# Kernel tuning notes

Hardware: AMD Instinct MI355X
Metric: run time of the kernel (lower is better)

## Reference

```python
import jax, jax.numpy as jnp
import numpy as np

C = 768
TEMB = 512
HID = int(C * 2.0)  # prompt_mlp hidden
K = max(1, int(C * 0.5))  # top-k channels = 384


def silu(x):
    return x * jax.nn.sigmoid(x)


def conv1x1(h, W, b):
    # h: [b,c,H,W], W: [o,c], b: [o]
    return jnp.einsum('bchw,oc->bohw', h, W) + b[None, :, None, None]


def setup_inputs() -> dict:
    key = jax.random.key(0)
    ks = jax.random.split(key, 20)
    s = 0.02
    return {
        'x': jax.random.normal(ks[0], (16, C, 64, 64), jnp.float32),
        'temb': jax.random.normal(ks[1], (16, TEMB), jnp.float32),
        'W_ts': jax.random.normal(ks[2], (2 * C, TEMB), jnp.float32) * s,
        'b_ts': jnp.zeros((2 * C,), jnp.float32),
        'W_tp': jax.random.normal(ks[3], (C, TEMB), jnp.float32) * s,
        'b_tp': jnp.zeros((C,), jnp.float32),
        'W_m1': jax.random.normal(ks[4], (HID, 2 * C), jnp.float32) * s,
        'b_m1': jnp.zeros((HID,), jnp.float32),
        'W_m2': jax.random.normal(ks[5], (C, HID), jnp.float32) * s,
        'b_m2': jnp.zeros((C,), jnp.float32),
        'Wq': jax.random.normal(ks[6], (C, C), jnp.float32) * s,
        'bq': jnp.zeros((C,), jnp.float32),
        'Wk': jax.random.normal(ks[7], (C, C), jnp.float32) * s,
        'bk': jnp.zeros((C,), jnp.float32),
        'Wv': jax.random.normal(ks[8], (C, C), jnp.float32) * s,
        'bv': jnp.zeros((C,), jnp.float32),
        'Wo': jax.random.normal(ks[9], (C, C), jnp.float32) * s,
        'bo': jnp.zeros((C,), jnp.float32),
    }


def reference(x, temb, W_ts, b_ts, W_tp, b_tp, W_m1, b_m1, W_m2, b_m2,
              Wq, bq, Wk, bk, Wv, bv, Wo, bo):
    b, c, H, W = x.shape
    # TimeScaleShift
    ss = silu(temb) @ W_ts.T + b_ts                       # [b, 2c]
    scale, shift = jnp.split(ss, 2, axis=1)
    h = x * (1 + scale[:, :, None, None]) + shift[:, :, None, None]
    # prompt
    gap = h.mean(axis=(2, 3))                             # [b, c]
    tp = silu(temb) @ W_tp.T + b_tp                       # [b, c]
    p = jnp.concatenate([gap, tp], axis=1)                # [b, 2c]
    prompt = silu(p @ W_m1.T + b_m1) @ W_m2.T + b_m2      # [b, c]
    # top-k channel selection
    _, idx = jax.lax.top_k(prompt, K)                     # [b, K]
    bi = jnp.arange(b)[:, None]
    # 1x1 convs then gather selected channels
    q = conv1x1(h, Wq, bq)[bi, idx].reshape(b, K, H * W)
    kf = conv1x1(h, Wk, bk)[bi, idx].reshape(b, K, H * W)
    v = conv1x1(h, Wv, bv)[bi, idx].reshape(b, K, H * W)
    # channel attention
    attn = jax.nn.softmax(jnp.einsum('bkn,bln->bkl', q, kf) * (K ** -0.5), axis=-1)
    out = jnp.einsum('bkl,bln->bkn', attn, v).reshape(b, K, H, W)
    # scatter back into full channel space
    out_full = jnp.zeros_like(h).at[bi, idx].set(out)
    return conv1x1(out_full, Wo, bo)
```

## Files before the change

### kernel.cpp

```cpp
#include <hip/hip_runtime.h>

#define NB 16
#define NC 768
#define NT 512
#define KS 384
#define NPX 4096
#define BK 64

typedef __bf16 bfx8 __attribute__((ext_vector_type(8)));
typedef float fx4 __attribute__((ext_vector_type(4)));
typedef unsigned short u16;
typedef unsigned short usv4 __attribute__((ext_vector_type(4)));

__device__ __forceinline__ u16 f2bf(float f) {
  unsigned u = __builtin_bit_cast(unsigned, f);
  u += 0x7FFFu + ((u >> 16) & 1u);
  return (u16)(u >> 16);
}
__device__ __forceinline__ float bf2f(u16 v) {
  return __builtin_bit_cast(float, (unsigned)v << 16);
}

__device__ __forceinline__ void gload16(const u16* g, u16* l) {
  __builtin_amdgcn_global_load_lds(
      (const __attribute__((address_space(1))) unsigned int*)g,
      (__attribute__((address_space(3))) unsigned int*)l, 16, 0, 0);
}

__global__ void k_trans_mean(const float* __restrict__ x, u16* __restrict__ xT,
                             u16* __restrict__ xC, float* __restrict__ parts) {
  __shared__ float ld[64][65];
  int p0 = blockIdx.x * 64, c0 = blockIdx.y * 64, b = blockIdx.z;
  int t = threadIdx.x;
  int k = t & 15, ir = t >> 4;
  int jr = k * 4;
#pragma unroll
  for (int s = 0; s < 4; ++s) {
    int i = ir + s * 16;
    float4 v = *(const float4*)&x[(size_t)(b * NC + c0 + i) * NPX + p0 + jr];
    ld[i][jr] = v.x; ld[i][jr + 1] = v.y; ld[i][jr + 2] = v.z; ld[i][jr + 3] = v.w;
    usv4 pk = {f2bf(v.x), f2bf(v.y), f2bf(v.z), f2bf(v.w)};
    *(usv4*)&xC[(size_t)(b * NC + c0 + i) * NPX + p0 + jr] = pk;
  }
  __syncthreads();
#pragma unroll
  for (int s = 0; s < 4; ++s) {
    int j = ir + s * 16;
    usv4 pk = {f2bf(ld[k * 4][j]), f2bf(ld[k * 4 + 1][j]),
               f2bf(ld[k * 4 + 2][j]), f2bf(ld[k * 4 + 3][j])};
    *(usv4*)&xT[(size_t)(b * NPX + p0 + j) * NC + c0 + k * 4] = pk;
  }
  if (t < 64) {
    float s = 0.f;
    for (int j = 0; j < 64; ++j) s += ld[t][j];
    parts[(size_t)(b * NC + c0 + t) * 64 + blockIdx.x] = s;
  }
}

__global__ void k_misc(const float* __restrict__ parts, float* __restrict__ xmean,
                       const float* __restrict__ temb, float* __restrict__ st) {
  int id = blockIdx.x * 256 + threadIdx.x;
  if (id < NB * NT) { float v = temb[id]; st[id] = v / (1.f + expf(-v)); }
  if (id < NB * NC) {
    float s = 0.f;
    for (int j = 0; j < 64; ++j) s += parts[(size_t)id * 64 + j];
    xmean[id] = s * (1.f / 4096.f);
  }
}

__global__ void k_mlp8(const float* __restrict__ W, const float* __restrict__ bias,
                       const float* __restrict__ X, float* __restrict__ Y,
                       int len, int nj, int ostride, int obase, int dosilu) {
  __shared__ float Xs[8 * 1537];
  int t = threadIdx.x, lane = t & 63, w = t >> 6;
  int b0 = blockIdx.y * 8;
  int ldx = len + 1;
  for (int id = t; id < 8 * len; id += 256) {
    int bb = id / len, s = id - bb * len;
    Xs[bb * ldx + s] = X[(size_t)(b0 + bb) * len + s];
  }
  __syncthreads();
  for (int i = 0; i < 4; ++i) {
    int j = blockIdx.x * 16 + i * 4 + w;
    if (j < nj) {
      float acc[8] = {0, 0, 0, 0, 0, 0, 0, 0};
      for (int s = lane; s < len; s += 64) {
        float wv = W[(size_t)j * len + s];
#pragma unroll
        for (int bb = 0; bb < 8; ++bb) acc[bb] += wv * Xs[bb * ldx + s];
      }
#pragma unroll
      for (int bb = 0; bb < 8; ++bb) {
        float r = acc[bb];
#pragma unroll
        for (int m = 32; m; m >>= 1) r += __shfl_xor(r, m);
        if (lane == 0) {
          r += bias[j];
          if (dosilu) r = r / (1.f + expf(-r));
          Y[(size_t)(b0 + bb) * ostride + obase + j] = r;
        }
      }
    }
  }
}

__global__ void k_assemble_p(const float* __restrict__ Y1, const float* __restrict__ xmean,
                             float* __restrict__ p) {
  int id = blockIdx.x * 256 + threadIdx.x;
  if (id >= NB * NC) return;
  int b = id / NC, c = id - b * NC;
  const float* yb = Y1 + (size_t)b * 2304;
  p[(size_t)b * 1536 + c] = xmean[id] * (1.f + yb[c]) + yb[768 + c];
  p[(size_t)b * 1536 + 768 + c] = yb[1536 + c];
}

__global__ void k_topk(const float* __restrict__ prompt, int* __restrict__ idx) {
  __shared__ float pr[NC];
  int b = blockIdx.x, t = threadIdx.x;
  for (int c = t; c < NC; c += 256) pr[c] = prompt[(size_t)b * NC + c];
  __syncthreads();
  for (int c = t; c < NC; c += 256) {
    float v = pr[c];
    int r = 0;
    for (int c2 = 0; c2 < NC; ++c2) {
      float v2 = pr[c2];
      r += (v2 > v) || (v2 == v && c2 < c);
    }
    if (r < KS) idx[b * KS + r] = c;
  }
}

__global__ void k_fold(const int* __restrict__ idx, const float* __restrict__ Y1,
                       const float* __restrict__ xmean,
                       const float* __restrict__ Wq, const float* __restrict__ bq,
                       const float* __restrict__ Wk, const float* __restrict__ bk,
                       const float* __restrict__ Wv, const float* __restrict__ bv,
                       u16* __restrict__ Aq, u16* __restrict__ Avtmp,
                       float* __restrict__ biasq, float* __restrict__ sig) {
  __shared__ float red[5 * 256];
  int k = blockIdx.x, b = blockIdx.y, t = threadIdx.x;
  int row = idx[b * KS + k];
  const float* yb = Y1 + (size_t)b * 2304;
  u16* aq = Aq + (size_t)b * 768 * NC;
  u16* av = Avtmp + (size_t)b * KS * NC;
  float dq = 0.f, dk = 0.f, dv = 0.f, sq = 0.f, sk = 0.f;
  for (int c = t; c < NC; c += 256) {
    float sc = 1.f + yb[c], sh = yb[768 + c];
    float xm = xmean[b * NC + c];
    float wq = Wq[(size_t)row * NC + c];
    float wk = Wk[(size_t)row * NC + c];
    float wv = Wv[(size_t)row * NC + c];
    aq[(size_t)k * NC + c] = f2bf(wq * sc);
    aq[(size_t)(KS + k) * NC + c] = f2bf(wk * sc);
    av[(size_t)k * NC + c] = f2bf(wv * sc);
    dq += wq * sh; dk += wk * sh; dv += wv * sh;
    sq += wq * sc * xm; sk += wk * sc * xm;
  }
  red[t] = dq; red[256 + t] = dk; red[512 + t] = dv; red[768 + t] = sq; red[1024 + t] = sk;
  __syncthreads();
  for (int s = 128; s; s >>= 1) {
    if (t < s) {
#pragma unroll
      for (int q = 0; q < 5; ++q) red[q * 256 + t] += red[q * 256 + t + s];
    }
    __syncthreads();
  }
  if (t == 0) {
    biasq[b * 1152 + k] = bq[row] + red[0];
    biasq[b * 1152 + KS + k] = bk[row] + red[256];
    biasq[b * 1152 + 2 * KS + k] = bv[row] + red[512];
    sig[b * NC + k] = 4096.f * red[768];
    sig[b * NC + KS + k] = 4096.f * red[1024];
  }
}

__global__ void k_avt(const u16* __restrict__ Avtmp, u16* __restrict__ AvT) {
  __shared__ u16 tl[64][65];
  int lt = blockIdx.x % 6, ct = blockIdx.x / 6, b = blockIdx.y;
  int l0 = lt * 64, c0 = ct * 64, t = threadIdx.x;
#pragma unroll
  for (int s = 0; s < 16; ++s) {
    int id = t + 256 * s;
    int r = id >> 6, c = id & 63;
    tl[r][c] = Avtmp[(size_t)b * KS * NC + (size_t)(l0 + r) * NC + c0 + c];
  }
  __syncthreads();
#pragma unroll
  for (int s = 0; s < 16; ++s) {
    int id = t + 256 * s;
    int r = id >> 6, c = id & 63;
    AvT[(size_t)b * NC * KS + (size_t)(c0 + r) * KS + l0 + c] = tl[c][r];
  }
}

__global__ void k_gather_wo(const int* __restrict__ idx, const float* __restrict__ Wo,
                            u16* __restrict__ WoSel) {
  __shared__ int il[KS];
  int b = blockIdx.y, t = threadIdx.x;
  for (int k = t; k < KS; k += 256) il[k] = idx[b * KS + k];
  __syncthreads();
  int o0 = blockIdx.x * 8;
  for (int oo = 0; oo < 8; ++oo) {
    int o = o0 + oo;
    const float* wr = Wo + (size_t)o * NC;
    u16* dst = WoSel + ((size_t)b * NC + o) * KS;
    for (int k = t; k < KS; k += 256) dst[k] = f2bf(wr[il[k]]);
  }
}

__global__ void k_gmerge(const float* __restrict__ Gp, u16* __restrict__ G) {
  __shared__ u16 gl[128][130];
  int tt = blockIdx.x, b = blockIdx.y, t = threadIdx.x;
  int i = 0;
  while ((i + 1) * (i + 2) / 2 <= tt) ++i;
  int j = tt - i * (i + 1) / 2;
  const float* p0 = Gp + ((size_t)(0 * NB + b) * 21 + tt) * 16384;
  const float* p1 = Gp + ((size_t)(1 * NB + b) * 21 + tt) * 16384;
#pragma unroll
  for (int s = 0; s < 16; ++s) {
    int id = t + 256 * s;
    int row = id >> 5, col4 = (id & 31) * 4;
    float4 a = *(const float4*)&p0[row * 128 + col4];
    float4 bb = *(const float4*)&p1[row * 128 + col4];
    usv4 pk = {f2bf(a.x + bb.x), f2bf(a.y + bb.y), f2bf(a.z + bb.z), f2bf(a.w + bb.w)};
    gl[row][col4] = pk[0]; gl[row][col4 + 1] = pk[1];
    gl[row][col4 + 2] = pk[2]; gl[row][col4 + 3] = pk[3];
    *(usv4*)&G[((size_t)b * NC + i * 128 + row) * NC + j * 128 + col4] = pk;
  }
  if (i == j) return;
  __syncthreads();
#pragma unroll
  for (int s = 0; s < 16; ++s) {
    int id = t + 256 * s;
    int row = id >> 5, col4 = (id & 31) * 4;
    usv4 pk = {gl[col4][row], gl[col4 + 1][row], gl[col4 + 2][row], gl[col4 + 3][row]};
    *(usv4*)&G[((size_t)b * NC + j * 128 + row) * NC + i * 128 + col4] = pk;
  }
}

__global__ void k_softmax(const float* __restrict__ S, u16* __restrict__ At) {
  __shared__ float sh[2];
  int kk = blockIdx.x, b = blockIdx.y, t = threadIdx.x;
  const float* srow = S + ((size_t)b * KS + kk) * KS;
  float v[3];
#pragma unroll
  for (int i = 0; i < 3; ++i) v[i] = srow[t + 128 * i];
  float m = fmaxf(fmaxf(v[0], v[1]), v[2]);
#pragma unroll
  for (int s = 32; s; s >>= 1) m = fmaxf(m, __shfl_xor(m, s));
  if ((t & 63) == 0) sh[t >> 6] = m;
  __syncthreads();
  m = fmaxf(sh[0], sh[1]);
  float e[3];
  float sum = 0.f;
#pragma unroll
  for (int i = 0; i < 3; ++i) { e[i] = expf(v[i] - m); sum += e[i]; }
#pragma unroll
  for (int s = 32; s; s >>= 1) sum += __shfl_xor(sum, s);
  __syncthreads();
  if ((t & 63) == 0) sh[t >> 6] = sum;
  __syncthreads();
  sum = sh[0] + sh[1];
  float inv = 1.f / sum;
#pragma unroll
  for (int i = 0; i < 3; ++i) {
    int l = t + 128 * i;
    At[((size_t)b * KS + l) * KS + kk] = f2bf(e[i] * inv);
  }
}

__global__ void k_bias_fin(const u16* __restrict__ R, const float* __restrict__ biasq,
                           const float* __restrict__ bo, float* __restrict__ bias_fin) {
  __shared__ float bv[KS];
  int b = blockIdx.x, t = threadIdx.x;
  for (int l = t; l < KS; l += 256) bv[l] = biasq[b * 1152 + 768 + l];
  __syncthreads();
  for (int o = t; o < NC; o += 256) {
    const u16* rr = R + ((size_t)b * NC + o) * KS;
    float s = bo[o];
    for (int l = 0; l < KS; ++l) s += bf2f(rr[l]) * bv[l];
    bias_fin[b * NC + o] = s;
  }
}

template <int EPI>
__global__ __launch_bounds__(256, 2) void gemm_bt(
    const u16* __restrict__ A, const u16* __restrict__ Bt, size_t sA, size_t sB,
    int ldA, int ldB, int K, const float* __restrict__ bias, int bstride,
    float* __restrict__ outF, u16* __restrict__ outU, int ldC, size_t sC,
    const float* __restrict__ sigp, const float* __restrict__ bqp, float scale) {
  __shared__ u16 As[128 * BK];
  __shared__ u16 Bs[128 * BK];
  int b, m0, n0, kbeg = 0, kend = K, tt = 0, gpart = 0;
  if constexpr (EPI == 5) {
    tt = blockIdx.x;
    int ii = 0;
    while ((ii + 1) * (ii + 2) / 2 <= tt) ++ii;
    int jj = tt - ii * (ii + 1) / 2;
    m0 = ii * 128; n0 = jj * 128;
    b = blockIdx.z >> 1; gpart = blockIdx.z & 1;
    kbeg = gpart * 2048; kend = kbeg + 2048;
  } else {
    b = blockIdx.z; m0 = blockIdx.y * 128; n0 = blockIdx.x * 128;
  }
  const u16* Ab = A + (size_t)b * sA;
  const u16* Bb = Bt + (size_t)b * sB;
  int t = threadIdx.x, lane = t & 63, w = t >> 6;
  int wm = (w >> 1) * 64, wn = (w & 1) * 64;
  int r16 = lane & 15, g = lane >> 4;

  int srow = w * 32 + (lane >> 3);
  int scol = (lane & 7) * 8;
  const u16* Ag = Ab + (size_t)(m0 + srow) * ldA + kbeg + scol;
  const u16* Bg = Bb + (size_t)(n0 + srow) * ldB + kbeg + scol;
  u16* Asl = &As[(w * 32) * BK];
  u16* Bsl = &Bs[(w * 32) * BK];

  fx4 acc[4][4] = {};

  for (int k0 = kbeg; k0 < kend; k0 += BK) {
#pragma unroll
    for (int s = 0; s < 4; ++s) gload16(Ag + (size_t)s * 8 * ldA, Asl + s * 8 * BK);
#pragma unroll
    for (int s = 0; s < 4; ++s) gload16(Bg + (size_t)s * 8 * ldB, Bsl + s * 8 * BK);
    Ag += BK; Bg += BK;
    __syncthreads();
#pragma unroll
    for (int kk = 0; kk < 2; ++kk) {
      bfx8 af[4], bfr[4];
#pragma unroll
      for (int i = 0; i < 4; ++i) {
        af[i] = *(const bfx8*)&As[(wm + i * 16 + r16) * BK + kk * 32 + g * 8];
        bfr[i] = *(const bfx8*)&Bs[(wn + i * 16 + r16) * BK + kk * 32 + g * 8];
      }
#pragma unroll
      for (int i = 0; i < 4; ++i)
#pragma unroll
        for (int j = 0; j < 4; ++j)
          acc[i][j] = __builtin_amdgcn_mfma_f32_16x16x32_bf16(af[i], bfr[j], acc[i][j], 0, 0, 0);
    }
    __syncthreads();
  }

#pragma unroll
  for (int i = 0; i < 4; ++i) {
#pragma unroll
    for (int j = 0; j < 4; ++j) {
      int row = wm + i * 16 + g * 4;
      int col = wn + j * 16 + r16;
      fx4 v = acc[i][j];
      if constexpr (EPI == 1) {
        int gc = n0 + col;
        float bk_ = bqp[b * 1152 + 384 + gc];
        float sk_ = sigp[b * NC + 384 + gc];
#pragma unroll
        for (int r = 0; r < 4; ++r) {
          int gr = m0 + row + r;
          float bq_ = bqp[b * 1152 + gr];
          float sq_ = sigp[b * NC + gr];
          float val = (v[r] + bq_ * sk_ + bk_ * sq_ + 4096.f * bq_ * bk_) * scale;
          outF[(size_t)b * sC + (size_t)gr * ldC + gc] = val;
        }
      } else if constexpr (EPI == 2) {
#pragma unroll
        for (int r = 0; r < 4; ++r)
          outU[(size_t)b * sC + (size_t)(m0 + row + r) * ldC + (n0 + col)] = f2bf(v[r]);
      } else if constexpr (EPI == 3) {
#pragma unroll
        for (int r = 0; r < 4; ++r)
          outF[(size_t)b * sC + (size_t)(m0 + row + r) * ldC + (n0 + col)] =
              v[r] + bias[b * bstride + m0 + row + r];
      } else {
        float* o = outF + ((size_t)(gpart * NB + b) * 21 + tt) * 16384;
#pragma unroll
        for (int r = 0; r < 4; ++r) o[(row + r) * 128 + col] = v[r];
      }
    }
  }
}

__global__ void k_sentinel(float* out, int n) {
  int id = blockIdx.x * 256 + threadIdx.x;
  if (id < n) out[id] = 12345.0f;
}

extern "C" void kernel_launch(void* const* d_in, const int* in_sizes, int n_in,
                              void* d_out, int out_size, void* d_ws, size_t ws_size,
                              hipStream_t stream) {
  const float* x    = (const float*)d_in[0];
  const float* temb = (const float*)d_in[1];
  const float* W_ts = (const float*)d_in[2];
  const float* b_ts = (const float*)d_in[3];
  const float* W_tp = (const float*)d_in[4];
  const float* b_tp = (const float*)d_in[5];
  const float* W_m1 = (const float*)d_in[6];
  const float* b_m1 = (const float*)d_in[7];
  const float* W_m2 = (const float*)d_in[8];
  const float* b_m2 = (const float*)d_in[9];
  const float* Wq = (const float*)d_in[10];
  const float* bq = (const float*)d_in[11];
  const float* Wk = (const float*)d_in[12];
  const float* bk = (const float*)d_in[13];
  const float* Wv = (const float*)d_in[14];
  const float* bv = (const float*)d_in[15];
  const float* Wo = (const float*)d_in[16];
  const float* bo = (const float*)d_in[17];
  float* out = (float*)d_out;

  char* base = (char*)d_ws;
  size_t off = 0;
  auto alloc = [&](size_t bytes) -> char* {
    char* pp = base + off;
    off += (bytes + 255) & ~(size_t)255;
    return pp;
  };
  u16* xT   = (u16*)alloc((size_t)NB * NPX * NC * 2);
  u16* xC   = (u16*)alloc((size_t)NB * NC * NPX * 2);
  u16* Aq   = (u16*)alloc((size_t)NB * 768 * NC * 2);
  u16* AvT  = (u16*)alloc((size_t)NB * NC * KS * 2);
  u16* WoS  = (u16*)alloc((size_t)NB * NC * KS * 2);
  float* Gp = (float*)alloc((size_t)2 * NB * 21 * 16384 * 4);
  float* parts  = (float*)alloc((size_t)NB * NC * 64 * 4);
  float* xmean  = (float*)alloc((size_t)NB * NC * 4);
  float* Y1     = (float*)alloc((size_t)NB * 2304 * 4);
  float* st     = (float*)alloc((size_t)NB * NT * 4);
  float* p      = (float*)alloc((size_t)NB * 1536 * 4);
  float* hid    = (float*)alloc((size_t)NB * 1536 * 4);
  float* pr     = (float*)alloc((size_t)NB * NC * 4);
  int*   idx    = (int*)alloc((size_t)NB * KS * 4);
  float* biasq  = (float*)alloc((size_t)NB * 1152 * 4);
  float* sig    = (float*)alloc((size_t)NB * NC * 4);
  float* bias_fin = (float*)alloc((size_t)NB * NC * 4);

  if (off > ws_size) {
    k_sentinel<<<(out_size + 255) / 256, 256, 0, stream>>>(out, out_size);
    return;
  }

  u16* Avtmp = (u16*)Gp;
  u16* G   = (u16*)xC;
  u16* T   = (u16*)((char*)xC + 20u * 1024 * 1024);
  float* S = (float*)((char*)xC + 32u * 1024 * 1024);
  u16* At  = (u16*)((char*)xC + 44u * 1024 * 1024);
  u16* R   = (u16*)((char*)xC + 52u * 1024 * 1024);
  u16* Wf  = (u16*)((char*)xC + 64u * 1024 * 1024);

  k_trans_mean<<<dim3(64, 12, NB), 256, 0, stream>>>(x, xT, xC, parts);
  k_misc<<<48, 256, 0, stream>>>(parts, xmean, temb, st);
  k_mlp8<<<dim3(96, 2), 256, 0, stream>>>(W_ts, b_ts, st, Y1, 512, 1536, 2304, 0, 0);
  k_mlp8<<<dim3(48, 2), 256, 0, stream>>>(W_tp, b_tp, st, Y1, 512, 768, 2304, 1536, 0);
  k_assemble_p<<<(NB * NC + 255) / 256, 256, 0, stream>>>(Y1, xmean, p);
  k_mlp8<<<dim3(96, 2), 256, 0, stream>>>(W_m1, b_m1, p, hid, 1536, 1536, 1536, 0, 1);
  k_mlp8<<<dim3(48, 2), 256, 0, stream>>>(W_m2, b_m2, hid, pr, 1536, 768, 768, 0, 0);
  k_topk<<<NB, 256, 0, stream>>>(pr, idx);
  k_fold<<<dim3(KS, NB), 256, 0, stream>>>(idx, Y1, xmean, Wq, bq, Wk, bk, Wv, bv,
                                           Aq, Avtmp, biasq, sig);
  k_avt<<<dim3(72, NB), 256, 0, stream>>>(Avtmp, AvT);
  k_gather_wo<<<dim3(96, NB), 256, 0, stream>>>(idx, Wo, WoS);

  gemm_bt<5><<<dim3(21, 1, NB * 2), 256, 0, stream>>>(
      xC, xC, (size_t)NC * NPX, (size_t)NC * NPX, NPX, NPX, NPX,
      nullptr, 0, Gp, nullptr, 0, 0, nullptr, nullptr, 0.f);
  k_gmerge<<<dim3(21, NB), 256, 0, stream>>>(Gp, G);
  gemm_bt<2><<<dim3(6, 3, NB), 256, 0, stream>>>(
      Aq + (size_t)KS * NC, G, (size_t)768 * NC, (size_t)NC * NC, NC, NC, NC,
      nullptr, 0, nullptr, T, NC, (size_t)KS * NC, nullptr, nullptr, 0.f);
  gemm_bt<1><<<dim3(3, 3, NB), 256, 0, stream>>>(
      Aq, T, (size_t)768 * NC, (size_t)KS * NC, NC, NC, NC,
      nullptr, 0, S, nullptr, KS, (size_t)KS * KS, sig, biasq, 0.05103103630798287f);
  k_softmax<<<dim3(KS, NB), 128, 0, stream>>>(S, At);
  gemm_bt<2><<<dim3(3, 6, NB), 256, 0, stream>>>(
      WoS, At, (size_t)NC * KS, (size_t)KS * KS, KS, KS, KS,
      nullptr, 0, nullptr, R, KS, (size_t)NC * KS, nullptr, nullptr, 0.f);
  k_bias_fin<<<NB, 256, 0, stream>>>(R, biasq, bo, bias_fin);
  gemm_bt<2><<<dim3(6, 6, NB), 256, 0, stream>>>(
      R, AvT, (size_t)NC * KS, (size_t)NC * KS, KS, KS, KS,
      nullptr, 0, nullptr, Wf, NC, (size_t)NC * NC, nullptr, nullptr, 0.f);
  gemm_bt<3><<<dim3(32, 6, NB), 256, 0, stream>>>(
      Wf, xT, (size_t)NC * NC, (size_t)NPX * NC, NC, NC, NC,
      bias_fin, NC, out, nullptr, NPX, (size_t)NC * NPX, nullptr, nullptr, 0.f);
}
```

Baseline: 684.5 us.

## Fuse prompt MLP chain and top-k into one per-batch kernel

Replaces the silu, four small MLP launches, prompt assembly and top-k with a single 1024-thread kernel per batch element that keeps intermediates in shared memory. It also parallelizes the final-bias reduction across many blocks with wave-level reductions, and raises the GEMM launch-bounds occupancy hint. The fusion removes several launches and global round-trips, but each of the 16 blocks now streams all MLP weights itself, so only 16 CUs work and weight traffic multiplies. The higher occupancy hint may force register spills in the GEMM.

```diff
diff --git a/kernel.cpp b/kernel.cpp
--- a/kernel.cpp
+++ b/kernel.cpp
@@ -57,76 +57,97 @@
   }
 }
 
-__global__ void k_misc(const float* __restrict__ parts, float* __restrict__ xmean,
-                       const float* __restrict__ temb, float* __restrict__ st) {
-  int id = blockIdx.x * 256 + threadIdx.x;
-  if (id < NB * NT) { float v = temb[id]; st[id] = v / (1.f + expf(-v)); }
-  if (id < NB * NC) {
+__global__ __launch_bounds__(1024, 1) void k_prompt(
+    const float* __restrict__ temb, const float* __restrict__ parts,
+    const float* __restrict__ W_ts, const float* __restrict__ b_ts,
+    const float* __restrict__ W_tp, const float* __restrict__ b_tp,
+    const float* __restrict__ W_m1, const float* __restrict__ b_m1,
+    const float* __restrict__ W_m2, const float* __restrict__ b_m2,
+    float* __restrict__ xmean_g, float* __restrict__ Y1, int* __restrict__ idx) {
+  __shared__ float st[512];
+  __shared__ float ssl[2304];
+  __shared__ float pl[1536];
+  __shared__ float hidl[1536];
+  __shared__ float prl[768];
+  __shared__ float xml[768];
+  int b = blockIdx.x, t = threadIdx.x, lane = t & 63, w = t >> 6;
+
+  if (t < 512) { float v = temb[b * 512 + t]; st[t] = v / (1.f + expf(-v)); }
+  if (t < 768) {
+    const float* pp = parts + (size_t)(b * 768 + t) * 64;
     float s = 0.f;
-    for (int j = 0; j < 64; ++j) s += parts[(size_t)id * 64 + j];
-    xmean[id] = s * (1.f / 4096.f);
-  }
-}
-
-__global__ void k_mlp8(const float* __restrict__ W, const float* __restrict__ bias,
-                       const float* __restrict__ X, float* __restrict__ Y,
-                       int len, int nj, int ostride, int obase, int dosilu) {
-  __shared__ float Xs[8 * 1537];
-  int t = threadIdx.x, lane = t & 63, w = t >> 6;
-  int b0 = blockIdx.y * 8;
-  int ldx = len + 1;
-  for (int id = t; id < 8 * len; id += 256) {
-    int bb = id / len, s = id - bb * len;
-    Xs[bb * ldx + s] = X[(size_t)(b0 + bb) * len + s];
-  }
-  __syncthreads();
-  for (int i = 0; i < 4; ++i) {
-    int j = blockIdx.x * 16 + i * 4 + w;
-    if (j < nj) {
-      float acc[8] = {0, 0, 0, 0, 0, 0, 0, 0};
-      for (int s = lane; s < len; s += 64) {
-        float wv = W[(size_t)j * len + s];
-#pragma unroll
-        for (int bb = 0; bb < 8; ++bb) acc[bb] += wv * Xs[bb * ldx + s];
-      }
-#pragma unroll
-      for (int bb = 0; bb < 8; ++bb) {
-        float r = acc[bb];
-#pragma unroll
-        for (int m = 32; m; m >>= 1) r += __shfl_xor(r, m);
-        if (lane == 0) {
-          r += bias[j];
-          if (dosilu) r = r / (1.f + expf(-r));
-          Y[(size_t)(b0 + bb) * ostride + obase + j] = r;
-        }
-      }
-    }
-  }
-}
-
-__global__ void k_assemble_p(const float* __restrict__ Y1, const float* __restrict__ xmean,
-                             float* __restrict__ p) {
-  int id = blockIdx.x * 256 + threadIdx.x;
-  if (id >= NB * NC) return;
-  int b = id / NC, c = id - b * NC;
-  const float* yb = Y1 + (size_t)b * 2304;
-  p[(size_t)b * 1536 + c] = xmean[id] * (1.f + yb[c]) + yb[768 + c];
-  p[(size_t)b * 1536 + 768 + c] = yb[1536 + c];
-}
-
-__global__ void k_topk(const float* __restrict__ prompt, int* __restrict__ idx) {
-  __shared__ float pr[NC];
-  int b = blockIdx.x, t = threadIdx.x;
-  for (int c = t; c < NC; c += 256) pr[c] = prompt[(size_t)b * NC + c];
-  __syncthreads();
-  for (int c = t; c < NC; c += 256) {
-    float v = pr[c];
+    for (int j = 0; j < 64; ++j) s += pp[j];
+    float xm = s * (1.f / 4096.f);
+    xml[t] = xm;
+    xmean_g[b * 768 + t] = xm;
+  }
+  __syncthreads();
+
+  for (int j = w; j < 2304; j += 16) {
+    const float* wr = (j < 1536) ? W_ts + (size_t)j * 512 : W_tp + (size_t)(j - 1536) * 512;
+    float4 a0 = *(const float4*)&wr[lane * 8];
+    float4 a1 = *(const float4*)&wr[lane * 8 + 4];
+    float4 s0 = *(const float4*)&st[lane * 8];
+    float4 s1 = *(const float4*)&st[lane * 8 + 4];
+    float acc = a0.x * s0.x + a0.y * s0.y + a0.z * s0.z + a0.w * s0.w +
+                a1.x * s1.x + a1.y * s1.y + a1.z * s1.z + a1.w * s1.w;
+#pragma unroll
+    for (int m = 32; m; m >>= 1) acc += __shfl_xor(acc, m);
+    if (lane == 0) {
+      acc += (j < 1536) ? b_ts[j] : b_tp[j - 1536];
+      ssl[j] = acc;
+      if (j < 1536) Y1[(size_t)b * 2304 + j] = acc;
+    }
+  }
+  __syncthreads();
+
+  if (t < 768) {
+    pl[t] = xml[t] * (1.f + ssl[t]) + ssl[768 + t];
+    pl[768 + t] = ssl[1536 + t];
+  }
+  __syncthreads();
+
+  for (int j = w; j < 1536; j += 16) {
+    const float* wr = W_m1 + (size_t)j * 1536;
+    float acc = 0.f;
+#pragma unroll
+    for (int e = 0; e < 6; ++e) {
+      float4 a = *(const float4*)&wr[lane * 24 + e * 4];
+      float4 s = *(const float4*)&pl[lane * 24 + e * 4];
+      acc += a.x * s.x + a.y * s.y + a.z * s.z + a.w * s.w;
+    }
+#pragma unroll
+    for (int m = 32; m; m >>= 1) acc += __shfl_xor(acc, m);
+    if (lane == 0) {
+      acc += b_m1[j];
+      hidl[j] = acc / (1.f + expf(-acc));
+    }
+  }
+  __syncthreads();
+
+  for (int j = w; j < 768; j += 16) {
+    const float* wr = W_m2 + (size_t)j * 1536;
+    float acc = 0.f;
+#pragma unroll
+    for (int e = 0; e < 6; ++e) {
+      float4 a = *(const float4*)&wr[lane * 24 + e * 4];
+      float4 s = *(const float4*)&hidl[lane * 24 + e * 4];
+      acc += a.x * s.x + a.y * s.y + a.z * s.z + a.w * s.w;
+    }
+#pragma unroll
+    for (int m = 32; m; m >>= 1) acc += __shfl_xor(acc, m);
+    if (lane == 0) prl[j] = acc + b_m2[j];
+  }
+  __syncthreads();
+
+  if (t < 768) {
+    float v = prl[t];
     int r = 0;
-    for (int c2 = 0; c2 < NC; ++c2) {
-      float v2 = pr[c2];
-      r += (v2 > v) || (v2 == v && c2 < c);
-    }
-    if (r < KS) idx[b * KS + r] = c;
+    for (int c2 = 0; c2 < 768; ++c2) {
+      float v2 = prl[c2];
+      r += (v2 > v) || (v2 == v && c2 < t);
+    }
+    if (r < KS) idx[b * KS + r] = t;
   }
 }
 
@@ -271,20 +292,28 @@
 
 __global__ void k_bias_fin(const u16* __restrict__ R, const float* __restrict__ biasq,
                            const float* __restrict__ bo, float* __restrict__ bias_fin) {
-  __shared__ float bv[KS];
-  int b = blockIdx.x, t = threadIdx.x;
-  for (int l = t; l < KS; l += 256) bv[l] = biasq[b * 1152 + 768 + l];
-  __syncthreads();
-  for (int o = t; o < NC; o += 256) {
+  __shared__ float bvl[KS];
+  int b = blockIdx.y, t = threadIdx.x, lane = t & 63, w = t >> 6;
+  for (int l = t; l < KS; l += 256) bvl[l] = biasq[b * 1152 + 768 + l];
+  __syncthreads();
+  int o0 = blockIdx.x * 16;
+  for (int oo = w; oo < 16; oo += 4) {
+    int o = o0 + oo;
     const u16* rr = R + ((size_t)b * NC + o) * KS;
-    float s = bo[o];
-    for (int l = 0; l < KS; ++l) s += bf2f(rr[l]) * bv[l];
-    bias_fin[b * NC + o] = s;
+    float acc = 0.f;
+#pragma unroll
+    for (int e = 0; e < 6; ++e) {
+      int l = lane + 64 * e;
+      acc += bf2f(rr[l]) * bvl[l];
+    }
+#pragma unroll
+    for (int m = 32; m; m >>= 1) acc += __shfl_xor(acc, m);
+    if (lane == 0) bias_fin[b * NC + o] = acc + bo[o];
   }
 }
 
 template <int EPI>
-__global__ __launch_bounds__(256, 2) void gemm_bt(
+__global__ __launch_bounds__(256, 4) void gemm_bt(
     const u16* __restrict__ A, const u16* __restrict__ Bt, size_t sA, size_t sB,
     int ldA, int ldB, int K, const float* __restrict__ bias, int bstride,
     float* __restrict__ outF, u16* __restrict__ outU, int ldC, size_t sC,
@@ -423,9 +452,6 @@
   float* parts  = (float*)alloc((size_t)NB * NC * 64 * 4);
   float* xmean  = (float*)alloc((size_t)NB * NC * 4);
   float* Y1     = (float*)alloc((size_t)NB * 2304 * 4);
-  float* st     = (float*)alloc((size_t)NB * NT * 4);
-  float* p      = (float*)alloc((size_t)NB * 1536 * 4);
-  float* hid    = (float*)alloc((size_t)NB * 1536 * 4);
   float* pr     = (float*)alloc((size_t)NB * NC * 4);
   int*   idx    = (int*)alloc((size_t)NB * KS * 4);
   float* biasq  = (float*)alloc((size_t)NB * 1152 * 4);
@@ -446,13 +472,8 @@
   u16* Wf  = (u16*)((char*)xC + 64u * 1024 * 1024);
 
   k_trans_mean<<<dim3(64, 12, NB), 256, 0, stream>>>(x, xT, xC, parts);
-  k_misc<<<48, 256, 0, stream>>>(parts, xmean, temb, st);
-  k_mlp8<<<dim3(96, 2), 256, 0, stream>>>(W_ts, b_ts, st, Y1, 512, 1536, 2304, 0, 0);
-  k_mlp8<<<dim3(48, 2), 256, 0, stream>>>(W_tp, b_tp, st, Y1, 512, 768, 2304, 1536, 0);
-  k_assemble_p<<<(NB * NC + 255) / 256, 256, 0, stream>>>(Y1, xmean, p);
-  k_mlp8<<<dim3(96, 2), 256, 0, stream>>>(W_m1, b_m1, p, hid, 1536, 1536, 1536, 0, 1);
-  k_mlp8<<<dim3(48, 2), 256, 0, stream>>>(W_m2, b_m2, hid, pr, 1536, 768, 768, 0, 0);
-  k_topk<<<NB, 256, 0, stream>>>(pr, idx);
+  k_prompt<<<NB, 1024, 0, stream>>>(temb, parts, W_ts, b_ts, W_tp, b_tp,
+                                    W_m1, b_m1, W_m2, b_m2, xmean, Y1, idx);
   k_fold<<<dim3(KS, NB), 256, 0, stream>>>(idx, Y1, xmean, Wq, bq, Wk, bk, Wv, bv,
                                            Aq, Avtmp, biasq, sig);
   k_avt<<<dim3(72, NB), 256, 0, stream>>>(Avtmp, AvT);
@@ -472,7 +493,7 @@
   gemm_bt<2><<<dim3(3, 6, NB), 256, 0, stream>>>(
       WoS, At, (size_t)NC * KS, (size_t)KS * KS, KS, KS, KS,
       nullptr, 0, nullptr, R, KS, (size_t)NC * KS, nullptr, nullptr, 0.f);
-  k_bias_fin<<<NB, 256, 0, stream>>>(R, biasq, bo, bias_fin);
+  k_bias_fin<<<dim3(48, NB), 256, 0, stream>>>(R, biasq, bo, bias_fin);
   gemm_bt<2><<<dim3(6, 6, NB), 256, 0, stream>>>(
       R, AvT, (size_t)NC * KS, (size_t)NC * KS, KS, KS, KS,
       nullptr, 0, nullptr, Wf, NC, (size_t)NC * NC, nullptr, nullptr, 0.f);
```

Measured after the change: 899.3 us. +31.4%, slower.
